# Optimization experiments

Measured on AMD Instinct MI355X. Metric: run time of the kernel, lower is better.

## Reference

```python
import jax, jax.numpy as jnp
import numpy as np

P_DROP = 0.7978529607897845  # dropout prob from source
N_HEADS = 25920              # fixed by Parameter shapes in __init__
S = 64
D = 64


def setup_inputs() -> dict:
    key = jax.random.key(0)
    k1, k2 = jax.random.split(key, 2)
    qt = jax.random.normal(k1, (N_HEADS, S, D), dtype=jnp.float32)
    k = jax.random.normal(k2, (N_HEADS, 1, D), dtype=jnp.float32)
    # learned parameters, sized exactly as in __init__
    biasb = jnp.zeros((N_HEADS, 1, 1), dtype=jnp.float32)
    scaleb = jnp.full((N_HEADS, 1, 1), 0.21, dtype=jnp.float32)
    return {"qt": qt, "k": k, "scaleb": scaleb, "biasb": biasb}


def reference(qt, k, scaleb, biasb):
    # a1 = qt @ k^T : (H,S,D) x (H,1,D) -> (H,S,1)
    a1 = jnp.einsum('hsd,htd->hst', qt, k)
    a2 = a1 * scaleb                       # learned per-head scale
    a3 = jax.nn.softmax(a2, axis=-1)       # softmax over singleton -> ones
    keep = 1.0 - P_DROP
    mask = jax.random.bernoulli(jax.random.key(42), keep, a3.shape)
    a4 = jnp.where(mask, a3 / keep, jnp.zeros((), a3.dtype))
    a5 = jnp.matmul(a4, biasb)             # (H,S,1) @ (H,1,1) -> (H,S,1)
    return a5 + qt                         # broadcast residual -> (H,S,D)
```

## Files before the change

kernel.cpp:

```cpp
#include <hip/hip_runtime.h>
#include <stdint.h>


#define NH 25920
#define NS 64
#define ND 64
#define HEADS_PER_BLOCK 4

typedef float f32x4 __attribute__((ext_vector_type(4)));

__device__ __forceinline__ uint32_t rotl32(uint32_t x, int n) {
  return (x << n) | (x >> (32 - n));
}

__device__ __forceinline__ void threefry2x32_0_42(uint32_t x0, uint32_t x1,
                                                  uint32_t& y0, uint32_t& y1) {
  const uint32_t ks0 = 0u;
  const uint32_t ks1 = 42u;
  const uint32_t ks2 = 0u ^ 42u ^ 0x1BD11BDAu;
  x0 += ks0; x1 += ks1;
#define RND(r) { x0 += x1; x1 = rotl32(x1, (r)); x1 ^= x0; }
  RND(13) RND(15) RND(26) RND(6)
  x0 += ks1; x1 += ks2 + 1u;
  RND(17) RND(29) RND(16) RND(24)
  x0 += ks2; x1 += ks0 + 2u;
  RND(13) RND(15) RND(26) RND(6)
  x0 += ks0; x1 += ks1 + 3u;
  RND(17) RND(29) RND(16) RND(24)
  x0 += ks1; x1 += ks2 + 4u;
  RND(13) RND(15) RND(26) RND(6)
  x0 += ks2; x1 += ks0 + 5u;
#undef RND
  y0 = x0; y1 = x1;
}

__global__ void __launch_bounds__(256)
fused_residual_kernel(const f32x4* __restrict__ qt4,
                      const float* __restrict__ biasb,
                      f32x4* __restrict__ out4) {
  const int h0 = blockIdx.x * HEADS_PER_BLOCK;
#pragma unroll
  for (int hh = 0; hh < HEADS_PER_BLOCK; ++hh) {
    const int h = h0 + hh;
    const float b = biasb[h];
    const int base = h << 10;
    if (b == 0.0f) {
#pragma unroll
      for (int j = 0; j < 4; ++j) {
        const int idx = base + (j << 8) + threadIdx.x;
        f32x4 v = __builtin_nontemporal_load(&qt4[idx]);
        __builtin_nontemporal_store(v, &out4[idx]);
      }
    } else {
      const float keep = 0.2021470392102155f;
#pragma unroll
      for (int j = 0; j < 4; ++j) {
        const int t = (j << 8) + threadIdx.x;
        const int idx = base + t;
        const uint32_t row = (uint32_t)((h << 6) + (t >> 4));
        const uint32_t n = (uint32_t)(NH * NS);
        const uint32_t half = n >> 1;
        uint32_t x0, x1, y0, y1;
        const bool hi = (row >= half);
        if (hi) { x0 = row - half; x1 = row; } else { x0 = row; x1 = row + half; }
        threefry2x32_0_42(x0, x1, y0, y1);
        const uint32_t bits = hi ? y1 : y0;
        const float u = __uint_as_float((bits >> 9) | 0x3F800000u) - 1.0f;
        const float add = (u < keep) ? (b / keep) : 0.0f;
        f32x4 v = __builtin_nontemporal_load(&qt4[idx]);
        v.x += add; v.y += add; v.z += add; v.w += add;
        __builtin_nontemporal_store(v, &out4[idx]);
      }
    }
  }
}

extern "C" void kernel_launch(void* const* d_in, const int* in_sizes, int n_in,
                              void* d_out, int out_size, void* d_ws, size_t ws_size,
                              hipStream_t stream) {
  const f32x4* qt4 = (const f32x4*)d_in[0];
  const float* biasb = (const float*)d_in[3];
  f32x4* out4 = (f32x4*)d_out;

  const int grid = NH / HEADS_PER_BLOCK;
  fused_residual_kernel<<<grid, 256, 0, stream>>>(qt4, biasb, out4);
}
```

Measured before the change: 150.6 us.

## Split into grid-stride bulk copy plus sparse dropout fixup kernel

Replaces the per-head fused kernel with a plain grid-stride copy kernel that streams qt into the output two vectors per iteration. A second kernel then, for heads with nonzero bias and rows the dropout mask keeps, adds the scaled bias in place. This decouples the bandwidth-bound copy from the per-head branch and RNG work, at the cost of an extra kernel launch and a read-modify-write pass over the kept rows.

```diff
diff --git a/kernel.cpp b/kernel.cpp
--- a/kernel.cpp
+++ b/kernel.cpp
@@ -5,7 +5,6 @@
 #define NH 25920
 #define NS 64
 #define ND 64
-#define HEADS_PER_BLOCK 4
 
 typedef float f32x4 __attribute__((ext_vector_type(4)));
 
@@ -35,43 +34,48 @@
 }
 
 __global__ void __launch_bounds__(256)
-fused_residual_kernel(const f32x4* __restrict__ qt4,
-                      const float* __restrict__ biasb,
-                      f32x4* __restrict__ out4) {
-  const int h0 = blockIdx.x * HEADS_PER_BLOCK;
+copy_kernel(const f32x4* __restrict__ src, f32x4* __restrict__ dst,
+            int total4) {
+  const int stride = gridDim.x * 256;
+  int i = blockIdx.x * 256 + threadIdx.x;
+  int i2 = i + stride;
+  for (; i2 < total4; i = i2 + stride, i2 = i + stride) {
+    f32x4 a = __builtin_nontemporal_load(src + i);
+    f32x4 b = __builtin_nontemporal_load(src + i2);
+    __builtin_nontemporal_store(a, dst + i);
+    __builtin_nontemporal_store(b, dst + i2);
+  }
+  if (i < total4) {
+    f32x4 a = __builtin_nontemporal_load(src + i);
+    __builtin_nontemporal_store(a, dst + i);
+  }
+}
+
+__global__ void __launch_bounds__(256)
+fixup_kernel(const float* __restrict__ biasb, f32x4* __restrict__ out4) {
+  const int wave = threadIdx.x >> 6;
+  const int lane = threadIdx.x & 63;
+  const int h = blockIdx.x * 4 + wave;
+  const float b = biasb[h];
+  if (b == 0.0f) return;
+  const float keep = 0.2021470392102155f;
+  const uint32_t row = (uint32_t)((h << 6) + lane);
+  const uint32_t n = (uint32_t)(NH * NS);
+  const uint32_t half = n >> 1;
+  uint32_t x0, x1, y0, y1;
+  const bool hi = (row >= half);
+  if (hi) { x0 = row - half; x1 = row; } else { x0 = row; x1 = row + half; }
+  threefry2x32_0_42(x0, x1, y0, y1);
+  const uint32_t bits = hi ? y1 : y0;
+  const float u = __uint_as_float((bits >> 9) | 0x3F800000u) - 1.0f;
+  if (u >= keep) return;
+  const float add = b / keep;
+  f32x4* p = out4 + ((h << 10) + (lane << 4));
 #pragma unroll
-  for (int hh = 0; hh < HEADS_PER_BLOCK; ++hh) {
-    const int h = h0 + hh;
-    const float b = biasb[h];
-    const int base = h << 10;
-    if (b == 0.0f) {
-#pragma unroll
-      for (int j = 0; j < 4; ++j) {
-        const int idx = base + (j << 8) + threadIdx.x;
-        f32x4 v = __builtin_nontemporal_load(&qt4[idx]);
-        __builtin_nontemporal_store(v, &out4[idx]);
-      }
-    } else {
-      const float keep = 0.2021470392102155f;
-#pragma unroll
-      for (int j = 0; j < 4; ++j) {
-        const int t = (j << 8) + threadIdx.x;
-        const int idx = base + t;
-        const uint32_t row = (uint32_t)((h << 6) + (t >> 4));
-        const uint32_t n = (uint32_t)(NH * NS);
-        const uint32_t half = n >> 1;
-        uint32_t x0, x1, y0, y1;
-        const bool hi = (row >= half);
-        if (hi) { x0 = row - half; x1 = row; } else { x0 = row; x1 = row + half; }
-        threefry2x32_0_42(x0, x1, y0, y1);
-        const uint32_t bits = hi ? y1 : y0;
-        const float u = __uint_as_float((bits >> 9) | 0x3F800000u) - 1.0f;
-        const float add = (u < keep) ? (b / keep) : 0.0f;
-        f32x4 v = __builtin_nontemporal_load(&qt4[idx]);
-        v.x += add; v.y += add; v.z += add; v.w += add;
-        __builtin_nontemporal_store(v, &out4[idx]);
-      }
-    }
+  for (int j = 0; j < 16; ++j) {
+    f32x4 v = p[j];
+    v.x += add; v.y += add; v.z += add; v.w += add;
+    p[j] = v;
   }
 }
 
@@ -82,6 +86,7 @@
   const float* biasb = (const float*)d_in[3];
   f32x4* out4 = (f32x4*)d_out;
 
-  const int grid = NH / HEADS_PER_BLOCK;
-  fused_residual_kernel<<<grid, 256, 0, stream>>>(qt4, biasb, out4);
+  const int total4 = (NH * NS * ND) / 4;
+  copy_kernel<<<5184, 256, 0, stream>>>(qt4, out4, total4);
+  fixup_kernel<<<NH / 4, 256, 0, stream>>>(biasb, out4);
 }
```

Result: slower. 158.9 us (+5.5%).
